# Performance work log

Hardware: AMD Instinct MI355X
Metric: run time of the kernel (lower is better)

## Reference

```python
import jax, jax.numpy as jnp
import numpy as np

EPSILON = 0.1
ALPHA = 0.5
N_ITER = 10
B, N, D, N_USERS = 4096, 4096, 16, 100000


def setup_inputs() -> dict:
    key = jax.random.key(0)
    k1, k2, k3, k4, k5, k6 = jax.random.split(key, 6)
    users_tensor = jax.random.randint(k1, (B,), 0, N_USERS)
    pois_tensor = jax.random.randint(k2, (B, N), 0, N)
    D_tensor = jax.random.uniform(k3, (B, N), dtype=jnp.float32)
    # ScaledEmbedding: normal init scaled by 1/embedding_dim
    poi_emb = jax.random.normal(k4, (N, D), dtype=jnp.float32) / D
    user_emb = jax.random.normal(k5, (N_USERS, D), dtype=jnp.float32) / D
    capacities = jax.random.uniform(k6, (N,), dtype=jnp.float32) + 0.5
    return {"users_tensor": users_tensor, "pois_tensor": pois_tensor,
            "D_tensor": D_tensor, "poi_emb": poi_emb,
            "user_emb": user_emb, "capacities": capacities}


def reference(users_tensor, pois_tensor, D_tensor, poi_emb, user_emb, capacities):
    pe = poi_emb[pois_tensor]            # [B, N, D]
    ue = user_emb[users_tensor]          # [B, D]
    dot = jnp.einsum('bnd,bd->bn', pe, ue)   # [B, N]
    affinity = (1.0 - ALPHA) * dot - ALPHA * (D_tensor / jnp.mean(D_tensor))
    K = jnp.exp(affinity / EPSILON)      # [B, N]
    a = jnp.ones((B,), dtype=K.dtype)
    b = capacities

    def body(i, uv):
        u, v = uv
        u = a / (K @ v)        # [B]
        v = b / (K.T @ u)      # [N]
        return (u, v)

    u0 = jnp.ones((B,), dtype=K.dtype)
    v0 = jnp.ones((N,), dtype=K.dtype)
    u, v = jax.lax.fori_loop(0, N_ITER, body, (u0, v0))
    P = K * (u[:, None] * v[None, :])    # [B, N]
    return P
```

## Files before the change

### kernel.cpp

```cpp
#include <hip/hip_runtime.h>
#include <hip/hip_fp16.h>

#define BB 4096
#define NN 4096
#define RPB 2

__global__ __launch_bounds__(256) void k_mean(
        const float* __restrict__ Dt, float* __restrict__ dsum,
        float* __restrict__ v) {
    const int tid = blockIdx.x * blockDim.x + threadIdx.x;
    if (tid < NN) v[tid] = 1.0f;
    const float4* D4 = (const float4*)Dt;
    const int total4 = (BB * NN) / 4;
    float s = 0.f;
    for (int i = tid; i < total4; i += gridDim.x * blockDim.x) {
        float4 d = D4[i];
        s += (d.x + d.y) + (d.z + d.w);
    }
    #pragma unroll
    for (int off = 32; off > 0; off >>= 1) s += __shfl_down(s, off, 64);
    __shared__ float ls[4];
    if ((threadIdx.x & 63) == 0) ls[threadIdx.x >> 6] = s;
    __syncthreads();
    if (threadIdx.x == 0) atomicAdd(dsum, (ls[0] + ls[1]) + (ls[2] + ls[3]));
}

__global__ __launch_bounds__(256) void k_K(
        const int* __restrict__ users, const int* __restrict__ pois,
        const float* __restrict__ Dt, const float* __restrict__ poi_emb,
        const float* __restrict__ user_emb, const float* __restrict__ dsum,
        __half* __restrict__ K) {
    __shared__ __half slut[RPB][NN];
    __shared__ float ues[RPB * 16];
    const int t = threadIdx.x;
    const int b0 = blockIdx.x * RPB;
    if (t < RPB * 16) {
        int r = t >> 4, d = t & 15;
        ues[t] = user_emb[(size_t)users[b0 + r] * 16 + d];
    }
    __syncthreads();
    float ue[RPB][16];
    #pragma unroll
    for (int r = 0; r < RPB; r++)
        #pragma unroll
        for (int d = 0; d < 16; d++) ue[r][d] = ues[r * 16 + d];

    const float4* pe4 = (const float4*)poi_emb;
    for (int j = t; j < NN; j += 256) {
        float4 p0 = pe4[j * 4 + 0];
        float4 p1 = pe4[j * 4 + 1];
        float4 p2 = pe4[j * 4 + 2];
        float4 p3 = pe4[j * 4 + 3];
        #pragma unroll
        for (int r = 0; r < RPB; r++) {
            float acc = p0.x*ue[r][0]  + p0.y*ue[r][1]  + p0.z*ue[r][2]  + p0.w*ue[r][3]
                      + p1.x*ue[r][4]  + p1.y*ue[r][5]  + p1.z*ue[r][6]  + p1.w*ue[r][7]
                      + p2.x*ue[r][8]  + p2.y*ue[r][9]  + p2.z*ue[r][10] + p2.w*ue[r][11]
                      + p3.x*ue[r][12] + p3.y*ue[r][13] + p3.z*ue[r][14] + p3.w*ue[r][15];
            slut[r][j] = __float2half(acc);
        }
    }
    __syncthreads();
    const float cc = 5.0f * 16777216.0f / dsum[0];
    #pragma unroll
    for (int r = 0; r < RPB; r++) {
        const size_t base = (size_t)(b0 + r) * NN;
        const int4*   p4 = (const int4*)(pois + base);
        const float4* d4 = (const float4*)(Dt + base);
        #pragma unroll
        for (int i = 0; i < NN / 4 / 256; i++) {
            const int q = t + i * 256;
            int4   ci = p4[q];
            float4 cd = d4[q];
            float k0 = __expf(5.0f * __half2float(slut[r][ci.x]) - cc * cd.x);
            float k1 = __expf(5.0f * __half2float(slut[r][ci.y]) - cc * cd.y);
            float k2 = __expf(5.0f * __half2float(slut[r][ci.z]) - cc * cd.z);
            float k3 = __expf(5.0f * __half2float(slut[r][ci.w]) - cc * cd.w);
            __half2* kw = (__half2*)&K[base + 4 * (size_t)q];
            kw[0] = __floats2half2_rn(k0, k1);
            kw[1] = __floats2half2_rn(k2, k3);
        }
    }
}

__global__ __launch_bounds__(256) void k_T(
        const __half* __restrict__ K, __half* __restrict__ KT) {
    __shared__ __half tile[64][72];
    const int t = threadIdx.x;
    const int r = t >> 2;
    const int q = t & 3;
    const int n0 = blockIdx.x * 64;
    const int b0 = blockIdx.y * 64;
    #pragma unroll
    for (int i = 0; i < 2; i++) {
        int cseg = (q + 4 * i) * 8;
        float4 f = *(const float4*)&K[(size_t)(b0 + r) * NN + n0 + cseg];
        *(float4*)&tile[r][cseg] = f;
    }
    __syncthreads();
    #pragma unroll
    for (int i = 0; i < 2; i++) {
        int cseg = (q + 4 * i) * 8;
        __half tmp[8];
        #pragma unroll
        for (int k = 0; k < 8; k++) tmp[k] = tile[cseg + k][r];
        *(float4*)&KT[(size_t)(n0 + r) * BB + b0 + cseg] = *(float4*)tmp;
    }
}

__device__ __forceinline__ float rowdot(const __half* __restrict__ row,
                                        const float* __restrict__ w, int t) {
    const float4* r4 = (const float4*)row;
    float4 h0 = r4[t], h1 = r4[256 + t];
    const __half2* a = (const __half2*)&h0;
    const __half2* b = (const __half2*)&h1;
    const float4* w4 = (const float4*)w;
    float4 wa0 = w4[2 * t], wa1 = w4[2 * t + 1];
    float4 wb0 = w4[512 + 2 * t], wb1 = w4[512 + 2 * t + 1];
    float s = 0.f; float2 f;
    f = __half22float2(a[0]); s += f.x * wa0.x + f.y * wa0.y;
    f = __half22float2(a[1]); s += f.x * wa0.z + f.y * wa0.w;
    f = __half22float2(a[2]); s += f.x * wa1.x + f.y * wa1.y;
    f = __half22float2(a[3]); s += f.x * wa1.z + f.y * wa1.w;
    f = __half22float2(b[0]); s += f.x * wb0.x + f.y * wb0.y;
    f = __half22float2(b[1]); s += f.x * wb0.z + f.y * wb0.w;
    f = __half22float2(b[2]); s += f.x * wb1.x + f.y * wb1.y;
    f = __half22float2(b[3]); s += f.x * wb1.z + f.y * wb1.w;
    #pragma unroll
    for (int off = 32; off > 0; off >>= 1) s += __shfl_down(s, off, 64);
    __shared__ float ls[4];
    if ((t & 63) == 0) ls[t >> 6] = s;
    __syncthreads();
    return (ls[0] + ls[1]) + (ls[2] + ls[3]);
}

__global__ __launch_bounds__(256) void k_u(
        const __half* __restrict__ K, const float* __restrict__ v,
        float* __restrict__ u) {
    float s = rowdot(K + (size_t)blockIdx.x * NN, v, threadIdx.x);
    if (threadIdx.x == 0) u[blockIdx.x] = 1.0f / s;
}

__global__ __launch_bounds__(256) void k_v(
        const __half* __restrict__ KT, const float* __restrict__ u,
        const float* __restrict__ cap, float* __restrict__ v) {
    float s = rowdot(KT + (size_t)blockIdx.x * BB, u, threadIdx.x);
    if (threadIdx.x == 0) v[blockIdx.x] = cap[blockIdx.x] / s;
}

__global__ __launch_bounds__(256) void k_P_h(
        const __half* __restrict__ K, const float* __restrict__ u,
        const float* __restrict__ v, float* __restrict__ P) {
    const int i = blockIdx.x * 256 + threadIdx.x;
    const int e = i * 8;
    const int b = e >> 12;
    const int col = e & 4095;
    float4 raw = ((const float4*)K)[i];
    const __half2* h = (const __half2*)&raw;
    const float ub = u[b];
    float4 v0 = ((const float4*)v)[col >> 2];
    float4 v1 = ((const float4*)v)[(col >> 2) + 1];
    float2 f0 = __half22float2(h[0]);
    float2 f1 = __half22float2(h[1]);
    float2 f2 = __half22float2(h[2]);
    float2 f3 = __half22float2(h[3]);
    ((float4*)P)[e >> 2]       = make_float4(f0.x*ub*v0.x, f0.y*ub*v0.y,
                                             f1.x*ub*v0.z, f1.y*ub*v0.w);
    ((float4*)P)[(e >> 2) + 1] = make_float4(f2.x*ub*v1.x, f2.y*ub*v1.y,
                                             f3.x*ub*v1.z, f3.y*ub*v1.w);
}

extern "C" void kernel_launch(void* const* d_in, const int* in_sizes, int n_in,
                              void* d_out, int out_size, void* d_ws, size_t ws_size,
                              hipStream_t stream) {
    const int*   users    = (const int*)d_in[0];
    const int*   pois     = (const int*)d_in[1];
    const float* Dt       = (const float*)d_in[2];
    const float* poi_emb  = (const float*)d_in[3];
    const float* user_emb = (const float*)d_in[4];
    const float* cap      = (const float*)d_in[5];
    float* out = (float*)d_out;

    float*  wsf  = (float*)d_ws;
    float*  dsum = wsf;
    float*  u    = wsf + 64;
    float*  v    = wsf + 64 + BB;
    __half* Kh   = (__half*)(wsf + 64 + BB + NN);
    __half* KT   = (__half*)d_out;

    hipMemsetAsync(dsum, 0, sizeof(float), stream);
    k_mean<<<2048, 256, 0, stream>>>(Dt, dsum, v);
    k_K<<<BB / RPB, 256, 0, stream>>>(users, pois, Dt, poi_emb, user_emb, dsum, Kh);
    k_T<<<dim3(NN / 64, BB / 64), 256, 0, stream>>>(Kh, KT);
    for (int it = 0; it < 10; it++) {
        k_u<<<BB, 256, 0, stream>>>(Kh, v, u);
        k_v<<<NN, 256, 0, stream>>>(KT, u, cap, v);
    }
    k_P_h<<<(BB * NN / 8) / 256, 256, 0, stream>>>(Kh, u, v, out);
}
```

Baseline: 393.0 us.

## Fuse Sinkhorn u and v updates into one pass over K with atomics

Drops the transposed copy of K and the separate u and v kernels. Each iteration now runs one kernel that computes u for 8 rows and, in the same pass over those rows, accumulates the K^T u column sums into replicated denominator buffers with atomics. v is recomputed on the fly as cap/den, and per-iteration buffers are zeroed upfront in k_mean so no memsets are needed between iterations. This halves K reads per iteration and removes the transpose, at the cost of many float atomics and nondeterministic summation order.

```diff
diff --git a/kernel.cpp b/kernel.cpp
--- a/kernel.cpp
+++ b/kernel.cpp
@@ -4,16 +4,22 @@
 #define BB 4096
 #define NN 4096
 #define RPB 2
+#define RPI 8
+#define NREP 2
+#define NSLICE 11
+#define DENF (NREP * NN)
 
 __global__ __launch_bounds__(256) void k_mean(
         const float* __restrict__ Dt, float* __restrict__ dsum,
-        float* __restrict__ v) {
+        float* __restrict__ den, const float* __restrict__ cap) {
     const int tid = blockIdx.x * blockDim.x + threadIdx.x;
-    if (tid < NN) v[tid] = 1.0f;
+    const int gs = gridDim.x * blockDim.x;
+    for (int i = tid; i < NSLICE * DENF; i += gs)
+        den[i] = (i < NN) ? cap[i] : 0.f;
     const float4* D4 = (const float4*)Dt;
     const int total4 = (BB * NN) / 4;
     float s = 0.f;
-    for (int i = tid; i < total4; i += gridDim.x * blockDim.x) {
+    for (int i = tid; i < total4; i += gs) {
         float4 d = D4[i];
         s += (d.x + d.y) + (d.z + d.w);
     }
@@ -83,40 +89,10 @@
     }
 }
 
-__global__ __launch_bounds__(256) void k_T(
-        const __half* __restrict__ K, __half* __restrict__ KT) {
-    __shared__ __half tile[64][72];
-    const int t = threadIdx.x;
-    const int r = t >> 2;
-    const int q = t & 3;
-    const int n0 = blockIdx.x * 64;
-    const int b0 = blockIdx.y * 64;
-    #pragma unroll
-    for (int i = 0; i < 2; i++) {
-        int cseg = (q + 4 * i) * 8;
-        float4 f = *(const float4*)&K[(size_t)(b0 + r) * NN + n0 + cseg];
-        *(float4*)&tile[r][cseg] = f;
-    }
-    __syncthreads();
-    #pragma unroll
-    for (int i = 0; i < 2; i++) {
-        int cseg = (q + 4 * i) * 8;
-        __half tmp[8];
-        #pragma unroll
-        for (int k = 0; k < 8; k++) tmp[k] = tile[cseg + k][r];
-        *(float4*)&KT[(size_t)(n0 + r) * BB + b0 + cseg] = *(float4*)tmp;
-    }
-}
-
-__device__ __forceinline__ float rowdot(const __half* __restrict__ row,
-                                        const float* __restrict__ w, int t) {
-    const float4* r4 = (const float4*)row;
-    float4 h0 = r4[t], h1 = r4[256 + t];
+__device__ __forceinline__ float dot16h(float4 h0, float4 h1,
+        float4 wa0, float4 wa1, float4 wb0, float4 wb1) {
     const __half2* a = (const __half2*)&h0;
     const __half2* b = (const __half2*)&h1;
-    const float4* w4 = (const float4*)w;
-    float4 wa0 = w4[2 * t], wa1 = w4[2 * t + 1];
-    float4 wb0 = w4[512 + 2 * t], wb1 = w4[512 + 2 * t + 1];
     float s = 0.f; float2 f;
     f = __half22float2(a[0]); s += f.x * wa0.x + f.y * wa0.y;
     f = __half22float2(a[1]); s += f.x * wa0.z + f.y * wa0.w;
@@ -126,48 +102,119 @@
     f = __half22float2(b[1]); s += f.x * wb0.z + f.y * wb0.w;
     f = __half22float2(b[2]); s += f.x * wb1.x + f.y * wb1.y;
     f = __half22float2(b[3]); s += f.x * wb1.z + f.y * wb1.w;
-    #pragma unroll
-    for (int off = 32; off > 0; off >>= 1) s += __shfl_down(s, off, 64);
-    __shared__ float ls[4];
-    if ((t & 63) == 0) ls[t >> 6] = s;
-    __syncthreads();
-    return (ls[0] + ls[1]) + (ls[2] + ls[3]);
-}
-
-__global__ __launch_bounds__(256) void k_u(
-        const __half* __restrict__ K, const float* __restrict__ v,
+    return s;
+}
+
+__global__ __launch_bounds__(256) void k_it(
+        const __half* __restrict__ K, const float* __restrict__ cap,
+        const float* __restrict__ denP, float* __restrict__ denN,
         float* __restrict__ u) {
-    float s = rowdot(K + (size_t)blockIdx.x * NN, v, threadIdx.x);
-    if (threadIdx.x == 0) u[blockIdx.x] = 1.0f / s;
-}
-
-__global__ __launch_bounds__(256) void k_v(
-        const __half* __restrict__ KT, const float* __restrict__ u,
-        const float* __restrict__ cap, float* __restrict__ v) {
-    float s = rowdot(KT + (size_t)blockIdx.x * BB, u, threadIdx.x);
-    if (threadIdx.x == 0) v[blockIdx.x] = cap[blockIdx.x] / s;
+    const int t = threadIdx.x;
+    const int r0 = blockIdx.x * RPI;
+
+    const float4* c4 = (const float4*)cap;
+    const float4* d4 = (const float4*)denP;
+    float4 ca0 = c4[2*t],       ca1 = c4[2*t+1];
+    float4 cb0 = c4[512+2*t],   cb1 = c4[512+2*t+1];
+    float4 da0 = d4[2*t],       da1 = d4[2*t+1];
+    float4 db0 = d4[512+2*t],   db1 = d4[512+2*t+1];
+    float4 ea0 = d4[1024+2*t],     ea1 = d4[1024+2*t+1];
+    float4 eb0 = d4[1024+512+2*t], eb1 = d4[1024+512+2*t+1];
+    float4 wa0 = make_float4(ca0.x/(da0.x+ea0.x), ca0.y/(da0.y+ea0.y),
+                             ca0.z/(da0.z+ea0.z), ca0.w/(da0.w+ea0.w));
+    float4 wa1 = make_float4(ca1.x/(da1.x+ea1.x), ca1.y/(da1.y+ea1.y),
+                             ca1.z/(da1.z+ea1.z), ca1.w/(da1.w+ea1.w));
+    float4 wb0 = make_float4(cb0.x/(db0.x+eb0.x), cb0.y/(db0.y+eb0.y),
+                             cb0.z/(db0.z+eb0.z), cb0.w/(db0.w+eb0.w));
+    float4 wb1 = make_float4(cb1.x/(db1.x+eb1.x), cb1.y/(db1.y+eb1.y),
+                             cb1.z/(db1.z+eb1.z), cb1.w/(db1.w+eb1.w));
+
+    float4 h0[RPI], h1[RPI];
+    #pragma unroll
+    for (int r = 0; r < RPI; r++) {
+        const float4* rr = (const float4*)(K + (size_t)(r0 + r) * NN);
+        h0[r] = rr[t];
+        h1[r] = rr[256 + t];
+    }
+    float acc[RPI];
+    #pragma unroll
+    for (int r = 0; r < RPI; r++) acc[r] = dot16h(h0[r], h1[r], wa0, wa1, wb0, wb1);
+    #pragma unroll
+    for (int off = 32; off > 0; off >>= 1)
+        #pragma unroll
+        for (int r = 0; r < RPI; r++) acc[r] += __shfl_down(acc[r], off, 64);
+    __shared__ float ls[4][RPI];
+    __shared__ float us[RPI];
+    if ((t & 63) == 0)
+        #pragma unroll
+        for (int r = 0; r < RPI; r++) ls[t >> 6][r] = acc[r];
+    __syncthreads();
+    if (t < RPI) {
+        float uu = 1.0f / ((ls[0][t] + ls[1][t]) + (ls[2][t] + ls[3][t]));
+        us[t] = uu;
+        u[r0 + t] = uu;
+    }
+    __syncthreads();
+
+    float4 A0 = make_float4(0,0,0,0), A1 = A0, B0 = A0, B1 = A0;
+    #pragma unroll
+    for (int r = 0; r < RPI; r++) {
+        const float ur = us[r];
+        const __half2* a = (const __half2*)&h0[r];
+        const __half2* b = (const __half2*)&h1[r];
+        float2 f;
+        f = __half22float2(a[0]); A0.x += ur*f.x; A0.y += ur*f.y;
+        f = __half22float2(a[1]); A0.z += ur*f.x; A0.w += ur*f.y;
+        f = __half22float2(a[2]); A1.x += ur*f.x; A1.y += ur*f.y;
+        f = __half22float2(a[3]); A1.z += ur*f.x; A1.w += ur*f.y;
+        f = __half22float2(b[0]); B0.x += ur*f.x; B0.y += ur*f.y;
+        f = __half22float2(b[1]); B0.z += ur*f.x; B0.w += ur*f.y;
+        f = __half22float2(b[2]); B1.x += ur*f.x; B1.y += ur*f.y;
+        f = __half22float2(b[3]); B1.z += ur*f.x; B1.w += ur*f.y;
+    }
+    float* dn = denN + (blockIdx.x & (NREP - 1)) * NN;
+    const int cA = 8 * t, cB = 2048 + 8 * t;
+    atomicAdd(&dn[cA+0], A0.x); atomicAdd(&dn[cA+1], A0.y);
+    atomicAdd(&dn[cA+2], A0.z); atomicAdd(&dn[cA+3], A0.w);
+    atomicAdd(&dn[cA+4], A1.x); atomicAdd(&dn[cA+5], A1.y);
+    atomicAdd(&dn[cA+6], A1.z); atomicAdd(&dn[cA+7], A1.w);
+    atomicAdd(&dn[cB+0], B0.x); atomicAdd(&dn[cB+1], B0.y);
+    atomicAdd(&dn[cB+2], B0.z); atomicAdd(&dn[cB+3], B0.w);
+    atomicAdd(&dn[cB+4], B1.x); atomicAdd(&dn[cB+5], B1.y);
+    atomicAdd(&dn[cB+6], B1.z); atomicAdd(&dn[cB+7], B1.w);
 }
 
 __global__ __launch_bounds__(256) void k_P_h(
         const __half* __restrict__ K, const float* __restrict__ u,
-        const float* __restrict__ v, float* __restrict__ P) {
-    const int i = blockIdx.x * 256 + threadIdx.x;
-    const int e = i * 8;
-    const int b = e >> 12;
-    const int col = e & 4095;
-    float4 raw = ((const float4*)K)[i];
-    const __half2* h = (const __half2*)&raw;
-    const float ub = u[b];
-    float4 v0 = ((const float4*)v)[col >> 2];
-    float4 v1 = ((const float4*)v)[(col >> 2) + 1];
-    float2 f0 = __half22float2(h[0]);
-    float2 f1 = __half22float2(h[1]);
-    float2 f2 = __half22float2(h[2]);
-    float2 f3 = __half22float2(h[3]);
-    ((float4*)P)[e >> 2]       = make_float4(f0.x*ub*v0.x, f0.y*ub*v0.y,
-                                             f1.x*ub*v0.z, f1.y*ub*v0.w);
-    ((float4*)P)[(e >> 2) + 1] = make_float4(f2.x*ub*v1.x, f2.y*ub*v1.y,
-                                             f3.x*ub*v1.z, f3.y*ub*v1.w);
+        const float* __restrict__ cap, const float* __restrict__ denF,
+        float* __restrict__ P) {
+    const int stride = gridDim.x * 256;
+    const float4* c4 = (const float4*)cap;
+    const float4* d4 = (const float4*)denF;
+    for (int i = blockIdx.x * 256 + threadIdx.x; i < BB * NN / 8; i += stride) {
+        const int e = i * 8;
+        const int b = e >> 12;
+        const int col = e & 4095;
+        const int q = col >> 2;
+        float4 raw = ((const float4*)K)[i];
+        const __half2* h = (const __half2*)&raw;
+        const float ub = u[b];
+        float4 c0 = c4[q], c1 = c4[q+1];
+        float4 d0 = d4[q], d1 = d4[q+1];
+        float4 e0 = d4[1024+q], e1 = d4[1024+q+1];
+        float4 v0 = make_float4(c0.x/(d0.x+e0.x), c0.y/(d0.y+e0.y),
+                                c0.z/(d0.z+e0.z), c0.w/(d0.w+e0.w));
+        float4 v1 = make_float4(c1.x/(d1.x+e1.x), c1.y/(d1.y+e1.y),
+                                c1.z/(d1.z+e1.z), c1.w/(d1.w+e1.w));
+        float2 f0 = __half22float2(h[0]);
+        float2 f1 = __half22float2(h[1]);
+        float2 f2 = __half22float2(h[2]);
+        float2 f3 = __half22float2(h[3]);
+        ((float4*)P)[e >> 2]       = make_float4(f0.x*ub*v0.x, f0.y*ub*v0.y,
+                                                 f1.x*ub*v0.z, f1.y*ub*v0.w);
+        ((float4*)P)[(e >> 2) + 1] = make_float4(f2.x*ub*v1.x, f2.y*ub*v1.y,
+                                                 f3.x*ub*v1.z, f3.y*ub*v1.w);
+    }
 }
 
 extern "C" void kernel_launch(void* const* d_in, const int* in_sizes, int n_in,
@@ -184,17 +231,15 @@
     float*  wsf  = (float*)d_ws;
     float*  dsum = wsf;
     float*  u    = wsf + 64;
-    float*  v    = wsf + 64 + BB;
-    __half* Kh   = (__half*)(wsf + 64 + BB + NN);
-    __half* KT   = (__half*)d_out;
+    float*  den  = wsf + 64 + BB;
+    __half* Kh   = (__half*)(den + NSLICE * DENF);
 
     hipMemsetAsync(dsum, 0, sizeof(float), stream);
-    k_mean<<<2048, 256, 0, stream>>>(Dt, dsum, v);
+    k_mean<<<2048, 256, 0, stream>>>(Dt, dsum, den, cap);
     k_K<<<BB / RPB, 256, 0, stream>>>(users, pois, Dt, poi_emb, user_emb, dsum, Kh);
-    k_T<<<dim3(NN / 64, BB / 64), 256, 0, stream>>>(Kh, KT);
     for (int it = 0; it < 10; it++) {
-        k_u<<<BB, 256, 0, stream>>>(Kh, v, u);
-        k_v<<<NN, 256, 0, stream>>>(KT, u, cap, v);
-    }
-    k_P_h<<<(BB * NN / 8) / 256, 256, 0, stream>>>(Kh, u, v, out);
-}
+        k_it<<<BB / RPI, 256, 0, stream>>>(Kh, cap, den + it * DENF,
+                                           den + (it + 1) * DENF, u);
+    }
+    k_P_h<<<2048, 256, 0, stream>>>(Kh, u, cap, den + 10 * DENF, out);
+}
```

Result: slower. 1.332 ms (+239.0%).
